# Kernel optimization log

Hardware: AMD Instinct MI355X
Metric: run time of the kernel (lower is better)

The kernel has to match this reference:

```python
import jax, jax.numpy as jnp
import numpy as np

LRELU_SLOPE = 0.2  # PyG GATConv default negative_slope
LN_EPS = 1e-5


def _layer_norm(x, g, b):
    mu = x.mean(-1, keepdims=True)
    var = x.var(-1, keepdims=True)
    return (x - mu) / jnp.sqrt(var + LN_EPS) * g + b


def _gat_conv(x, src, dst, W, a_src, a_dst, bias, heads, out_c, concat):
    # PyG GATConv (eval mode, self-loops already appended to src/dst).
    N = x.shape[0]
    h = (x @ W).reshape(N, heads, out_c)            # [N,H,C]
    e_src = (h * a_src).sum(-1)                     # [N,H]
    e_dst = (h * a_dst).sum(-1)                     # [N,H]
    e = jax.nn.leaky_relu(e_src[src] + e_dst[dst], LRELU_SLOPE)  # [E,H]
    # segment softmax over incoming edges of each dst node
    m = jax.ops.segment_max(e, dst, num_segments=N)
    m = jnp.where(jnp.isfinite(m), m, 0.0)
    w = jnp.exp(e - m[dst])
    denom = jax.ops.segment_sum(w, dst, num_segments=N)
    alpha = w / (denom[dst] + 1e-16)                # [E,H]
    out = jax.ops.segment_sum(h[src] * alpha[:, :, None], dst, num_segments=N)  # [N,H,C]
    out = out.reshape(N, heads * out_c) if concat else out.mean(1)
    return out + bias


def setup_inputs() -> dict:
    key = jax.random.key(0)
    ks = jax.random.split(key, 16)
    N, E, F0, Hd, H, G = 50000, 800000, 32, 32, 4, 512
    s = 0.1
    nrm = lambda k, shape: jax.random.normal(k, shape, jnp.float32) * s
    d = {}
    d['x'] = jax.random.normal(ks[0], (N, F0), jnp.float32)
    d['edge_index'] = jax.random.randint(ks[1], (2, E), 0, N)
    d['batch'] = jnp.sort(jax.random.randint(ks[2], (N,), 0, G))
    d['num_graphs'] = G
    # layer 1: F0 -> (Hd, H heads, concat)
    d['W1'] = nrm(ks[3], (F0, H * Hd)); d['as1'] = nrm(ks[4], (H, Hd)); d['ad1'] = nrm(ks[5], (H, Hd))
    d['b1'] = jnp.zeros((H * Hd,)); d['g1'] = jnp.ones((H * Hd,)); d['be1'] = jnp.zeros((H * Hd,))
    # layer 2: H*Hd -> (Hd, H heads, concat)
    d['W2'] = nrm(ks[6], (H * Hd, H * Hd)); d['as2'] = nrm(ks[7], (H, Hd)); d['ad2'] = nrm(ks[8], (H, Hd))
    d['b2'] = jnp.zeros((H * Hd,)); d['g2'] = jnp.ones((H * Hd,)); d['be2'] = jnp.zeros((H * Hd,))
    # layer 3: H*Hd -> (Hd, 1 head, mean)
    d['W3'] = nrm(ks[9], (H * Hd, Hd)); d['as3'] = nrm(ks[10], (1, Hd)); d['ad3'] = nrm(ks[11], (1, Hd))
    d['b3'] = jnp.zeros((Hd,)); d['g3'] = jnp.ones((Hd,)); d['be3'] = jnp.zeros((Hd,))
    # classifier MLP: 2*Hd -> Hd -> Hd//2 -> 1 (torch Linear [out,in])
    d['cW1'] = nrm(ks[12], (Hd, 2 * Hd)); d['cb1'] = jnp.zeros((Hd,))
    d['cW2'] = nrm(ks[13], (Hd // 2, Hd)); d['cb2'] = jnp.zeros((Hd // 2,))
    d['cW3'] = nrm(ks[14], (1, Hd // 2)); d['cb3'] = jnp.zeros((1,))
    return d


def reference(x, edge_index, batch, num_graphs,
              W1, as1, ad1, b1, g1, be1,
              W2, as2, ad2, b2, g2, be2,
              W3, as3, ad3, b3, g3, be3,
              cW1, cb1, cW2, cb2, cW3, cb3):
    N = x.shape[0]
    loop = jnp.arange(N)
    src = jnp.concatenate([edge_index[0], loop])
    dst = jnp.concatenate([edge_index[1], loop])
    h = jax.nn.elu(_layer_norm(_gat_conv(x, src, dst, W1, as1, ad1, b1, 4, 32, True), g1, be1))
    h = jax.nn.elu(_layer_norm(_gat_conv(h, src, dst, W2, as2, ad2, b2, 4, 32, True), g2, be2))
    h = jax.nn.elu(_layer_norm(_gat_conv(h, src, dst, W3, as3, ad3, b3, 1, 32, False), g3, be3))
    cnt = jax.ops.segment_sum(jnp.ones((N,), h.dtype), batch, num_segments=num_graphs)
    x_mean = jax.ops.segment_sum(h, batch, num_segments=num_graphs) / jnp.maximum(cnt, 1.0)[:, None]
    x_max = jax.ops.segment_max(h, batch, num_segments=num_graphs)
    f = jnp.concatenate([x_mean, x_max], axis=1)        # [G, 64]
    f = jax.nn.relu(f @ cW1.T + cb1)
    f = jax.nn.relu(f @ cW2.T + cb2)
    return (f @ cW3.T + cb3).squeeze(-1)                 # [G]
```

## Files before the change

kernel.cpp:

```cpp
#include <hip/hip_runtime.h>
#include <hip/hip_fp16.h>
#include <math.h>

#define CDIV(a, b) (((a) + (b) - 1) / (b))
#define SCAN_BS 1024
#define NBUK 512
#define ATILE 4096

typedef _Float16 f16x8 __attribute__((ext_vector_type(8)));
typedef float f32x4 __attribute__((ext_vector_type(4)));

__device__ __forceinline__ unsigned encf(float v) {
    unsigned u = __float_as_uint(v);
    return (u & 0x80000000u) ? ~u : (u | 0x80000000u);
}
__device__ __forceinline__ float decf(unsigned k) {
    unsigned u = (k & 0x80000000u) ? (k ^ 0x80000000u) : ~k;
    return __uint_as_float(u);
}

__device__ __forceinline__ float lrelu(float v) {
    return v > 0.f ? v : 0.2f * v;
}

__global__ __launch_bounds__(256) void gemm_kernel(
    const float* __restrict__ X, const float* __restrict__ W,
    float* __restrict__ Y, int M, int K, int Nout) {
    int idx = blockIdx.x * blockDim.x + threadIdx.x;
    if (idx >= M * Nout) return;
    int row = idx / Nout;
    int col = idx - row * Nout;
    const float* xr = X + (size_t)row * K;
    const float* wc = W + col;
    float acc = 0.f;
    for (int k = 0; k < K; k += 4) {
        float4 xv = *(const float4*)(xr + k);
        acc += xv.x * wc[(size_t)(k + 0) * Nout];
        acc += xv.y * wc[(size_t)(k + 1) * Nout];
        acc += xv.z * wc[(size_t)(k + 2) * Nout];
        acc += xv.w * wc[(size_t)(k + 3) * Nout];
    }
    Y[idx] = acc;
}

__device__ __forceinline__ void wprep_one(const float* __restrict__ W,
                                          __half* __restrict__ Whf, int K,
                                          int NOUT, int idx) {
    int NK = K / 32;
    int l = idx & 63, f = idx >> 6;
    int ks = f % NK, tt = f / NK;
    int quad = l >> 4, c15 = l & 15;
    _Float16 v[8];
#pragma unroll
    for (int j = 0; j < 8; ++j) {
        int k = ks * 32 + quad * 8 + j;
        int n = tt * 16 + c15;
        v[j] = (_Float16)W[(size_t)k * NOUT + n];
    }
    *(uint4*)(Whf + (size_t)idx * 8) = *(uint4*)v;
}

__device__ __forceinline__ void wprep_one_lds(const float* __restrict__ W,
                                              __half* Whf, int K, int NOUT,
                                              int idx) {
    int NK = K / 32;
    int l = idx & 63, f = idx >> 6;
    int ks = f % NK, tt = f / NK;
    int quad = l >> 4, c15 = l & 15;
    _Float16 v[8];
#pragma unroll
    for (int j = 0; j < 8; ++j) {
        int k = ks * 32 + quad * 8 + j;
        int n = tt * 16 + c15;
        v[j] = (_Float16)W[(size_t)k * NOUT + n];
    }
    *(uint4*)(Whf + (size_t)idx * 8) = *(uint4*)v;
}

__device__ __forceinline__ f16x8 loadA(const float* p) {
    float4 lo = *(const float4*)p;
    float4 hi = *(const float4*)(p + 4);
    f16x8 a;
    a[0] = (_Float16)lo.x; a[1] = (_Float16)lo.y;
    a[2] = (_Float16)lo.z; a[3] = (_Float16)lo.w;
    a[4] = (_Float16)hi.x; a[5] = (_Float16)hi.y;
    a[6] = (_Float16)hi.z; a[7] = (_Float16)hi.w;
    return a;
}
__device__ __forceinline__ f16x8 loadA(const __half* p) {
    return *(const f16x8*)p;
}

template <int K, int NOUT, int HH, typename XT, typename BP>
__device__ __forceinline__ void gemm_attn_body(
    const XT* __restrict__ X, const BP* bp, __half* __restrict__ Y,
    const float* __restrict__ a_src, const float* __restrict__ a_dst,
    float* __restrict__ es, float* __restrict__ ed, int M, int blk) {
    constexpr int NK = K / 32, NT = NOUT / 16;
    static_assert(NT == 2 * HH, "32 channels per head assumed");
    int wave = threadIdx.x >> 6, lane = threadIdx.x & 63;
    int quad = lane >> 4, c15 = lane & 15;
    int row0 = (blk * 4 + wave) * 16;
    if (row0 >= M) return;
    int arow = row0 + c15;
    if (arow >= M) arow = M - 1;
    const XT* xr = X + (size_t)arow * K + quad * 8;
    f32x4 acc[NT];
#pragma unroll
    for (int t = 0; t < NT; ++t) {
        acc[t][0] = 0.f; acc[t][1] = 0.f; acc[t][2] = 0.f; acc[t][3] = 0.f;
    }
#pragma unroll
    for (int ks = 0; ks < NK; ++ks) {
        f16x8 a = loadA(xr + ks * 32);
#pragma unroll
        for (int t = 0; t < NT; ++t) {
            f16x8 b = *(const f16x8*)&bp[((t * NK + ks) * 64 + lane) * 8];
            acc[t] = __builtin_amdgcn_mfma_f32_16x16x32_f16(a, b, acc[t],
                                                            0, 0, 0);
        }
    }
#pragma unroll
    for (int r = 0; r < 4; ++r) {
        int row = row0 + quad * 4 + r;
        if (row < M) {
#pragma unroll
            for (int t = 0; t < NT; ++t)
                Y[(size_t)row * NOUT + t * 16 + c15] = (__half)acc[t][r];
        }
    }
    float asv[NT], adv[NT];
#pragma unroll
    for (int t = 0; t < NT; ++t) {
        asv[t] = a_src[t * 16 + c15];
        adv[t] = a_dst[t * 16 + c15];
    }
#pragma unroll
    for (int h = 0; h < HH; ++h) {
#pragma unroll
        for (int r = 0; r < 4; ++r) {
            float s = acc[2 * h][r] * asv[2 * h] +
                      acc[2 * h + 1][r] * asv[2 * h + 1];
            float dd = acc[2 * h][r] * adv[2 * h] +
                       acc[2 * h + 1][r] * adv[2 * h + 1];
#pragma unroll
            for (int off = 8; off >= 1; off >>= 1) {
                s += __shfl_xor(s, off);
                dd += __shfl_xor(dd, off);
            }
            int row = row0 + quad * 4 + r;
            if (row < M) {
                if (c15 == 0) es[row * HH + h] = s;
                if (c15 == 1) ed[row * HH + h] = dd;
            }
        }
    }
}

template <int K, int NOUT, int HH, typename XT>
__global__ __launch_bounds__(256) void gemm_mfma_attn(
    const XT* __restrict__ X, const __half* __restrict__ Whf,
    __half* __restrict__ Y, const float* __restrict__ a_src,
    const float* __restrict__ a_dst, float* __restrict__ es,
    float* __restrict__ ed, int M) {
    gemm_attn_body<K, NOUT, HH>(X, Whf, Y, a_src, a_dst, es, ed, M,
                                blockIdx.x);
}

__global__ __launch_bounds__(256) void binA1_kernel(
    const int* __restrict__ ei, int E, int* __restrict__ ghist,
    int* __restrict__ pool0, int poolN, const float* __restrict__ W1,
    const float* __restrict__ W2, const float* __restrict__ W3,
    __half* __restrict__ wh2, __half* __restrict__ wh3,
    int* __restrict__ rowptr, int N, int nhist, int nwp,
    const float* __restrict__ x, __half* __restrict__ Qh,
    const float* __restrict__ as1, const float* __restrict__ ad1,
    float* __restrict__ es, float* __restrict__ ed) {
    __shared__ int lh[NBUK];
    __shared__ __half wlds[512 * 8];
    int t = threadIdx.x;
    if (blockIdx.x >= nhist + nwp) {
        for (int i = t; i < 512; i += 256)
            wprep_one_lds(W1, wlds, 32, 128, i);
        __syncthreads();
        gemm_attn_body<32, 128, 4>(x, wlds, Qh, as1, ad1, es, ed, N,
                                   blockIdx.x - nhist - nwp);
        return;
    }
    if (blockIdx.x >= nhist) {
        int idx = (blockIdx.x - nhist) * 256 + t;
        if (idx == 0) rowptr[N] = E + N;
        if (idx < 2048) {
            wprep_one(W2, wh2, 128, 128, idx);
        } else if (idx < 2560) {
            wprep_one(W3, wh3, 128, 32, idx - 2048);
        }
        return;
    }
    int gid = blockIdx.x * 256 + t;
    if (gid < poolN) pool0[gid] = 0;
    for (int i = t; i < NBUK; i += 256) lh[i] = 0;
    __syncthreads();
    int base = blockIdx.x * ATILE;
#pragma unroll 4
    for (int j = 0; j < ATILE / 256; ++j) {
        int idx = base + t + 256 * j;
        if (idx < E) atomicAdd(&lh[ei[E + idx] >> 7], 1);
    }
    __syncthreads();
    int* gh = ghist + (size_t)blockIdx.x * NBUK;
    for (int i = t; i < NBUK; i += 256) gh[i] = lh[i];
}

__global__ __launch_bounds__(64) void binA2a_kernel(
    int* __restrict__ ghist, int* __restrict__ tot, int nblk) {
    int b = blockIdx.x;
    int lane = threadIdx.x;
    int accb = 0;
    for (int chunk = 0; chunk < nblk; chunk += 64) {
        int i = chunk + lane;
        int v = (i < nblk) ? ghist[(size_t)i * NBUK + b] : 0;
        int s = v;
        for (int off = 1; off < 64; off <<= 1) {
            int tv = __shfl_up(s, off);
            if (lane >= off) s += tv;
        }
        if (i < nblk) ghist[(size_t)i * NBUK + b] = s - v + accb;
        accb += __shfl(s, 63);
    }
    if (lane == 0) tot[b] = accb;
}

__device__ __forceinline__ void bucketScan(const int* __restrict__ tot,
                                           int* __restrict__ sc, int t,
                                           int& a0, int& a1, int& excl) {
    a0 = tot[2 * t];
    a1 = tot[2 * t + 1];
    int pair = a0 + a1;
    sc[t] = pair;
    __syncthreads();
#pragma unroll
    for (int off = 1; off < 256; off <<= 1) {
        int v = (t >= off) ? sc[t - off] : 0;
        __syncthreads();
        sc[t] += v;
        __syncthreads();
    }
    excl = sc[t] - pair;
}

__global__ __launch_bounds__(256) void binA3_kernel(
    const int* __restrict__ ei, int E, const int* __restrict__ ghist,
    const int* __restrict__ tot, unsigned* __restrict__ ebuf) {
    __shared__ int lcur[NBUK];
    __shared__ int sc[256];
    int t = threadIdx.x;
    int a0, a1, excl;
    bucketScan(tot, sc, t, a0, a1, excl);
    const int* gh = ghist + (size_t)blockIdx.x * NBUK;
    lcur[2 * t] = gh[2 * t] + excl;
    lcur[2 * t + 1] = gh[2 * t + 1] + excl + a0;
    __syncthreads();
    int base = blockIdx.x * ATILE;
#pragma unroll 4
    for (int j = 0; j < ATILE / 256; ++j) {
        int idx = base + t + 256 * j;
        if (idx < E) {
            int s = ei[idx];
            int d = ei[E + idx];
            int pos = atomicAdd(&lcur[d >> 7], 1);
            ebuf[pos] = ((unsigned)d << 16) | (unsigned)s;
        }
    }
}

__global__ __launch_bounds__(256) void binB_kernel(
    const unsigned* __restrict__ ebuf, const int* __restrict__ tot,
    int* __restrict__ rowptr, int* __restrict__ csrc, int N) {
    __shared__ int cnt_[128];
    __shared__ int pre[128];
    __shared__ int lcur[128];
    __shared__ int sc[256];
    __shared__ int begS;
    int b = blockIdx.x;
    int t = threadIdx.x;
    int n0 = b << 7;
    int totb = tot[b];
    if (t < 128) cnt_[t] = 0;
    int a0, a1, excl;
    bucketScan(tot, sc, t, a0, a1, excl);
    if (t == (b >> 1)) begS = (b & 1) ? (excl + a0) : excl;
    __syncthreads();
    int beg = begS, end = begS + totb;
    for (int i = beg + t; i < end; i += 256)
        atomicAdd(&cnt_[(ebuf[i] >> 16) - n0], 1);
    __syncthreads();
    if (t < 128) pre[t] = (n0 + t < N) ? (cnt_[t] + 1) : 0;
    __syncthreads();
    for (int off = 1; off < 128; off <<= 1) {
        int v = 0;
        if (t < 128 && t >= off) v = pre[t - off];
        __syncthreads();
        if (t < 128) pre[t] += v;
        __syncthreads();
    }
    int cbase = beg + n0;
    if (t < 128 && n0 + t < N) {
        int ex = pre[t] - (cnt_[t] + 1);
        int rp = cbase + ex;
        rowptr[n0 + t] = rp;
        csrc[rp] = n0 + t;
        lcur[t] = rp + 1;
    }
    __syncthreads();
    for (int i = beg + t; i < end; i += 256) {
        unsigned e = ebuf[i];
        int d = (int)(e >> 16) - n0;
        int s = (int)(e & 0xFFFFu);
        int pos = atomicAdd(&lcur[d], 1);
        csrc[pos] = s;
    }
}

__global__ __launch_bounds__(256) void attn_kernel(
    const float* __restrict__ h, const float* __restrict__ a_src,
    const float* __restrict__ a_dst, float* __restrict__ es,
    float* __restrict__ ed, int N, int H, int C) {
    int idx = blockIdx.x * blockDim.x + threadIdx.x;
    if (idx >= N * H) return;
    int n = idx / H;
    int hh = idx - n * H;
    const float* hp = h + (size_t)n * H * C + (size_t)hh * C;
    const float* ap = a_src + hh * C;
    const float* bp = a_dst + hh * C;
    float s = 0.f, d = 0.f;
    for (int c = 0; c < C; c += 4) {
        float4 hv = *(const float4*)(hp + c);
        float4 av = *(const float4*)(ap + c);
        float4 bv = *(const float4*)(bp + c);
        s += hv.x * av.x + hv.y * av.y + hv.z * av.z + hv.w * av.w;
        d += hv.x * bv.x + hv.y * bv.y + hv.z * bv.z + hv.w * bv.w;
    }
    es[idx] = s;
    ed[idx] = d;
}

__global__ __launch_bounds__(256) void deg_kernel(const int* __restrict__ ei,
                                                  int E,
                                                  int* __restrict__ deg) {
    int e = blockIdx.x * blockDim.x + threadIdx.x;
    if (e >= E) return;
    atomicAdd(&deg[ei[E + e]], 1);
}

__global__ __launch_bounds__(SCAN_BS) void scan1_kernel(
    const int* __restrict__ deg, int* __restrict__ rowptr,
    int* __restrict__ bsum, int N) {
    __shared__ int tmp[SCAN_BS];
    int tid = threadIdx.x;
    int gid = blockIdx.x * SCAN_BS + tid;
    int v = (gid < N) ? (deg[gid] + 1) : 0;
    tmp[tid] = v;
    __syncthreads();
    for (int off = 1; off < SCAN_BS; off <<= 1) {
        int t = (tid >= off) ? tmp[tid - off] : 0;
        __syncthreads();
        tmp[tid] += t;
        __syncthreads();
    }
    if (gid < N) rowptr[gid] = tmp[tid] - v;
    if (tid == SCAN_BS - 1) bsum[blockIdx.x] = tmp[tid];
}

__global__ void scan2_kernel(int* __restrict__ bsum, int nb) {
    if (threadIdx.x == 0 && blockIdx.x == 0) {
        int acc = 0;
        for (int i = 0; i < nb; ++i) {
            int t = bsum[i];
            bsum[i] = acc;
            acc += t;
        }
    }
}

__global__ __launch_bounds__(SCAN_BS) void scan3_kernel(
    int* __restrict__ rowptr, int* __restrict__ cursor,
    int* __restrict__ csrc, const int* __restrict__ bsum, int N, int total) {
    int gid = blockIdx.x * SCAN_BS + threadIdx.x;
    if (gid < N) {
        int v = rowptr[gid] + bsum[blockIdx.x];
        rowptr[gid] = v;
        cursor[gid] = v + 1;
        csrc[v] = gid;
    }
    if (gid == 0) rowptr[N] = total;
}

__global__ __launch_bounds__(256) void scatter_kernel(
    const int* __restrict__ ei, int E, int* __restrict__ cursor,
    int* __restrict__ csrc) {
    int e = blockIdx.x * blockDim.x + threadIdx.x;
    if (e >= E) return;
    int s = ei[e];
    int d = ei[E + e];
    int pos = atomicAdd(&cursor[d], 1);
    csrc[pos] = s;
}

__global__ __launch_bounds__(256) void aggr_ln128_kernel(
    const int* __restrict__ rowptr, const int* __restrict__ csrc,
    const __half* __restrict__ h, const float* __restrict__ es,
    const float* __restrict__ ed, const float* __restrict__ bias,
    const float* __restrict__ gam, const float* __restrict__ bet,
    __half* __restrict__ outp, int N) {
    constexpr int D = 128, H = 4;
    int d = (blockIdx.x * blockDim.x + threadIdx.x) >> 4;
    int cl = threadIdx.x & 15;
    if (d >= N) return;
    int c = cl * 8;
    int hh = cl >> 2;
    float edv = ed[d * H + hh];
    float acc[8];
#pragma unroll
    for (int i = 0; i < 8; ++i) acc[i] = 0.f;
    float l = 0.f;
    int k = rowptr[d], end = rowptr[d + 1];
    for (; k + 8 <= end; k += 8) {
        int s[8];
#pragma unroll
        for (int j = 0; j < 8; ++j) s[j] = csrc[k + j];
        float e[8];
#pragma unroll
        for (int j = 0; j < 8; ++j) e[j] = es[s[j] * H + hh];
        uint4 u[8];
#pragma unroll
        for (int j = 0; j < 8; ++j)
            u[j] = *(const uint4*)(h + (size_t)s[j] * D + c);
#pragma unroll
        for (int j = 0; j < 8; ++j) {
            float w = __expf(lrelu(e[j] + edv));
            l += w;
            const __half2* hp = (const __half2*)&u[j];
#pragma unroll
            for (int i = 0; i < 4; ++i) {
                float2 f = __half22float2(hp[i]);
                acc[2 * i] += w * f.x;
                acc[2 * i + 1] += w * f.y;
            }
        }
    }
    for (; k + 4 <= end; k += 4) {
        int s[4];
#pragma unroll
        for (int j = 0; j < 4; ++j) s[j] = csrc[k + j];
        float e[4];
#pragma unroll
        for (int j = 0; j < 4; ++j) e[j] = es[s[j] * H + hh];
        uint4 u[4];
#pragma unroll
        for (int j = 0; j < 4; ++j)
            u[j] = *(const uint4*)(h + (size_t)s[j] * D + c);
#pragma unroll
        for (int j = 0; j < 4; ++j) {
            float w = __expf(lrelu(e[j] + edv));
            l += w;
            const __half2* hp = (const __half2*)&u[j];
#pragma unroll
            for (int i = 0; i < 4; ++i) {
                float2 f = __half22float2(hp[i]);
                acc[2 * i] += w * f.x;
                acc[2 * i + 1] += w * f.y;
            }
        }
    }
    for (; k < end; ++k) {
        int s = csrc[k];
        float w = __expf(lrelu(es[s * H + hh] + edv));
        uint4 u = *(const uint4*)(h + (size_t)s * D + c);
        l += w;
        const __half2* hp = (const __half2*)&u;
#pragma unroll
        for (int i = 0; i < 4; ++i) {
            float2 f = __half22float2(hp[i]);
            acc[2 * i] += w * f.x;
            acc[2 * i + 1] += w * f.y;
        }
    }
    float rl = 1.f / (l + 1e-16f);
    float4 b0 = *(const float4*)(bias + c);
    float4 b1 = *(const float4*)(bias + c + 4);
    float v[8];
    v[0] = acc[0] * rl + b0.x; v[1] = acc[1] * rl + b0.y;
    v[2] = acc[2] * rl + b0.z; v[3] = acc[3] * rl + b0.w;
    v[4] = acc[4] * rl + b1.x; v[5] = acc[5] * rl + b1.y;
    v[6] = acc[6] * rl + b1.z; v[7] = acc[7] * rl + b1.w;
    float sm = 0.f, ssum = 0.f;
#pragma unroll
    for (int i = 0; i < 8; ++i) { sm += v[i]; ssum += v[i] * v[i]; }
#pragma unroll
    for (int off = 1; off <= 8; off <<= 1) {
        sm += __shfl_xor(sm, off);
        ssum += __shfl_xor(ssum, off);
    }
    float mean = sm / D;
    float var = ssum / D - mean * mean;
    float rstd = rsqrtf(var + 1e-5f);
    float4 g0 = *(const float4*)(gam + c);
    float4 g1 = *(const float4*)(gam + c + 4);
    float4 t0 = *(const float4*)(bet + c);
    float4 t1 = *(const float4*)(bet + c + 4);
    float gv[8] = {g0.x, g0.y, g0.z, g0.w, g1.x, g1.y, g1.z, g1.w};
    float tv[8] = {t0.x, t0.y, t0.z, t0.w, t1.x, t1.y, t1.z, t1.w};
    __half2 p[4];
#pragma unroll
    for (int i = 0; i < 4; ++i) {
        float o0 = (v[2 * i] - mean) * rstd * gv[2 * i] + tv[2 * i];
        float o1 = (v[2 * i + 1] - mean) * rstd * gv[2 * i + 1] + tv[2 * i + 1];
        o0 = o0 > 0.f ? o0 : expm1f(o0);
        o1 = o1 > 0.f ? o1 : expm1f(o1);
        p[i] = __floats2half2_rn(o0, o1);
    }
    uint4 uo;
    uo.x = *(unsigned*)&p[0];
    uo.y = *(unsigned*)&p[1];
    uo.z = *(unsigned*)&p[2];
    uo.w = *(unsigned*)&p[3];
    *(uint4*)(outp + (size_t)d * D + c) = uo;
}

__global__ __launch_bounds__(256) void aggr_ln32_pool_kernel(
    const int* __restrict__ rowptr, const int* __restrict__ csrc,
    const __half* __restrict__ h, const float* __restrict__ es,
    const float* __restrict__ ed, const float* __restrict__ bias,
    const float* __restrict__ gam, const float* __restrict__ bet,
    const int* __restrict__ batch, float* __restrict__ psum,
    unsigned* __restrict__ pmax, float* __restrict__ cnt, int N) {
    constexpr int D = 32;
    __shared__ float lsum[2][32];
    __shared__ unsigned lmax[2][32];
    __shared__ float lcnt[2];
    __shared__ int g0s;
    int tid = threadIdx.x;
    int d = (blockIdx.x * 256 + tid) >> 3;
    int cl = tid & 7;
    int c = cl * 4;
    int dbase = blockIdx.x * 32;
    if (tid < 64) {
        lsum[tid >> 5][tid & 31] = 0.f;
        lmax[tid >> 5][tid & 31] = 0u;
    }
    if (tid < 2) lcnt[tid] = 0.f;
    if (tid == 0) g0s = batch[dbase < N ? dbase : (N - 1)];
    __syncthreads();
    int g0 = g0s;
    if (d < N) {
        float edv = ed[d];
        float acc[4] = {0.f, 0.f, 0.f, 0.f};
        float l = 0.f;
        int k = rowptr[d], end = rowptr[d + 1];
        for (; k + 8 <= end; k += 8) {
            int s[8];
#pragma unroll
            for (int j = 0; j < 8; ++j) s[j] = csrc[k + j];
            float e[8];
#pragma unroll
            for (int j = 0; j < 8; ++j) e[j] = es[s[j]];
            uint2 u[8];
#pragma unroll
            for (int j = 0; j < 8; ++j)
                u[j] = *(const uint2*)(h + (size_t)s[j] * D + c);
#pragma unroll
            for (int j = 0; j < 8; ++j) {
                float w = __expf(lrelu(e[j] + edv));
                l += w;
                float2 f0 = __half22float2(*(__half2*)&u[j].x);
                float2 f1 = __half22float2(*(__half2*)&u[j].y);
                acc[0] += w * f0.x; acc[1] += w * f0.y;
                acc[2] += w * f1.x; acc[3] += w * f1.y;
            }
        }
        for (; k + 4 <= end; k += 4) {
            int s[4];
#pragma unroll
            for (int j = 0; j < 4; ++j) s[j] = csrc[k + j];
            float e[4];
#pragma unroll
            for (int j = 0; j < 4; ++j) e[j] = es[s[j]];
            uint2 u[4];
#pragma unroll
            for (int j = 0; j < 4; ++j)
                u[j] = *(const uint2*)(h + (size_t)s[j] * D + c);
#pragma unroll
            for (int j = 0; j < 4; ++j) {
                float w = __expf(lrelu(e[j] + edv));
                l += w;
                float2 f0 = __half22float2(*(__half2*)&u[j].x);
                float2 f1 = __half22float2(*(__half2*)&u[j].y);
                acc[0] += w * f0.x; acc[1] += w * f0.y;
                acc[2] += w * f1.x; acc[3] += w * f1.y;
            }
        }
        for (; k < end; ++k) {
            int s = csrc[k];
            float w = __expf(lrelu(es[s] + edv));
            uint2 u = *(const uint2*)(h + (size_t)s * D + c);
            l += w;
            float2 f0 = __half22float2(*(__half2*)&u.x);
            float2 f1 = __half22float2(*(__half2*)&u.y);
            acc[0] += w * f0.x; acc[1] += w * f0.y;
            acc[2] += w * f1.x; acc[3] += w * f1.y;
        }
        float rl = 1.f / (l + 1e-16f);
        float4 b4 = *(const float4*)(bias + c);
        float v0 = acc[0] * rl + b4.x;
        float v1 = acc[1] * rl + b4.y;
        float v2 = acc[2] * rl + b4.z;
        float v3 = acc[3] * rl + b4.w;
        float sm = v0 + v1 + v2 + v3;
        float ssum = v0 * v0 + v1 * v1 + v2 * v2 + v3 * v3;
#pragma unroll
        for (int off = 1; off <= 4; off <<= 1) {
            sm += __shfl_xor(sm, off);
            ssum += __shfl_xor(ssum, off);
        }
        float mean = sm / D;
        float var = ssum / D - mean * mean;
        float rstd = rsqrtf(var + 1e-5f);
        float4 g4 = *(const float4*)(gam + c);
        float4 t4 = *(const float4*)(bet + c);
        float o0 = (v0 - mean) * rstd * g4.x + t4.x;
        float o1 = (v1 - mean) * rstd * g4.y + t4.y;
        float o2 = (v2 - mean) * rstd * g4.z + t4.z;
        float o3 = (v3 - mean) * rstd * g4.w + t4.w;
        o0 = o0 > 0.f ? o0 : expm1f(o0);
        o1 = o1 > 0.f ? o1 : expm1f(o1);
        o2 = o2 > 0.f ? o2 : expm1f(o2);
        o3 = o3 > 0.f ? o3 : expm1f(o3);
        int g = batch[d];
        int goff = g - g0;
        if (goff >= 0 && goff < 2) {
            atomicAdd(&lsum[goff][c + 0], o0);
            atomicAdd(&lsum[goff][c + 1], o1);
            atomicAdd(&lsum[goff][c + 2], o2);
            atomicAdd(&lsum[goff][c + 3], o3);
            atomicMax(&lmax[goff][c + 0], encf(o0));
            atomicMax(&lmax[goff][c + 1], encf(o1));
            atomicMax(&lmax[goff][c + 2], encf(o2));
            atomicMax(&lmax[goff][c + 3], encf(o3));
            if (cl == 0) atomicAdd(&lcnt[goff], 1.0f);
        } else {
            atomicAdd(&psum[g * D + c + 0], o0);
            atomicAdd(&psum[g * D + c + 1], o1);
            atomicAdd(&psum[g * D + c + 2], o2);
            atomicAdd(&psum[g * D + c + 3], o3);
            atomicMax(&pmax[g * D + c + 0], encf(o0));
            atomicMax(&pmax[g * D + c + 1], encf(o1));
            atomicMax(&pmax[g * D + c + 2], encf(o2));
            atomicMax(&pmax[g * D + c + 3], encf(o3));
            if (cl == 0) atomicAdd(&cnt[g], 1.0f);
        }
    }
    __syncthreads();
    if (tid < 64) {
        int go = tid >> 5, cc = tid & 31;
        unsigned m = lmax[go][cc];
        if (m != 0u) {
            int gg = g0 + go;
            atomicAdd(&psum[gg * D + cc], lsum[go][cc]);
            atomicMax(&pmax[gg * D + cc], m);
            if (cc == 0) atomicAdd(&cnt[gg], lcnt[go]);
        }
    }
}

__global__ __launch_bounds__(256) void aggr_csr_kernel(
    const int* __restrict__ rowptr, const int* __restrict__ csrc,
    const float* __restrict__ h, const float* __restrict__ es,
    const float* __restrict__ ed, float* __restrict__ outp, int N, int H,
    int C) {
    int D = H * C;
    int wave = (blockIdx.x * blockDim.x + threadIdx.x) >> 6;
    int lane = threadIdx.x & 63;
    if (wave >= N) return;
    int d = wave;
    int c0 = lane, c1 = lane + 64;
    bool a0 = c0 < D, a1 = c1 < D;
    int h0 = a0 ? c0 / C : 0;
    int h1 = a1 ? c1 / C : 0;
    float edv0 = a0 ? ed[d * H + h0] : 0.f;
    float edv1 = a1 ? ed[d * H + h1] : 0.f;
    float m0 = -INFINITY, m1 = -INFINITY;
    float l0 = 0.f, l1 = 0.f, acc0 = 0.f, acc1 = 0.f;
    int beg = rowptr[d], end = rowptr[d + 1];
    for (int k = beg; k < end; ++k) {
        int s = csrc[k];
        const float* hp = h + (size_t)s * D;
        if (a0) {
            float v = lrelu(es[s * H + h0] + edv0);
            float nm = fmaxf(m0, v);
            float sc = __expf(m0 - nm);
            float w = __expf(v - nm);
            l0 = l0 * sc + w;
            acc0 = acc0 * sc + w * hp[c0];
            m0 = nm;
        }
        if (a1) {
            float v = lrelu(es[s * H + h1] + edv1);
            float nm = fmaxf(m1, v);
            float sc = __expf(m1 - nm);
            float w = __expf(v - nm);
            l1 = l1 * sc + w;
            acc1 = acc1 * sc + w * hp[c1];
            m1 = nm;
        }
    }
    if (a0) outp[(size_t)d * D + c0] = acc0 / (l0 + 1e-16f);
    if (a1) outp[(size_t)d * D + c1] = acc1 / (l1 + 1e-16f);
}

__global__ __launch_bounds__(64) void ln_elu_kernel(
    const float* __restrict__ in, const float* __restrict__ bias,
    const float* __restrict__ gam, const float* __restrict__ bet,
    float* __restrict__ outp, int D) {
    int n = blockIdx.x;
    int lane = threadIdx.x;
    int c0 = lane, c1 = lane + 64;
    bool a0 = c0 < D, a1 = c1 < D;
    float v0 = 0.f, v1 = 0.f;
    if (a0) v0 = in[(size_t)n * D + c0] + bias[c0];
    if (a1) v1 = in[(size_t)n * D + c1] + bias[c1];
    float s = v0 + v1;
    float ss = v0 * v0 + v1 * v1;
    for (int off = 32; off; off >>= 1) {
        s += __shfl_xor(s, off);
        ss += __shfl_xor(ss, off);
    }
    float mean = s / D;
    float var = ss / D - mean * mean;
    float rstd = rsqrtf(var + 1e-5f);
    if (a0) {
        float o = (v0 - mean) * rstd * gam[c0] + bet[c0];
        outp[(size_t)n * D + c0] = o > 0.f ? o : expm1f(o);
    }
    if (a1) {
        float o = (v1 - mean) * rstd * gam[c1] + bet[c1];
        outp[(size_t)n * D + c1] = o > 0.f ? o : expm1f(o);
    }
}

__global__ __launch_bounds__(256) void pool_kernel(
    const float* __restrict__ h, const int* __restrict__ batch, int N, int C,
    float* __restrict__ psum, unsigned* __restrict__ pmax,
    float* __restrict__ cnt) {
    int idx = blockIdx.x * blockDim.x + threadIdx.x;
    if (idx >= N * C) return;
    int n = idx / C;
    int c = idx - n * C;
    int g = batch[n];
    float v = h[(size_t)n * C + c];
    atomicAdd(&psum[g * C + c], v);
    atomicMax(&pmax[g * C + c], encf(v));
    if (c == 0) atomicAdd(&cnt[g], 1.0f);
}

__global__ __launch_bounds__(64) void mlp_kernel(
    const float* __restrict__ psum, const unsigned* __restrict__ pmax,
    const float* __restrict__ cnt, const float* __restrict__ cW1,
    const float* __restrict__ cb1, const float* __restrict__ cW2,
    const float* __restrict__ cb2, const float* __restrict__ cW3,
    const float* __restrict__ cb3, float* __restrict__ outp, int C) {
    __shared__ float f[64];
    __shared__ float t1[32];
    __shared__ float t2[16];
    int g = blockIdx.x;
    int t = threadIdx.x;
    float c = fmaxf(cnt[g], 1.0f);
    if (t < C) {
        f[t] = psum[g * C + t] / c;
    } else if (t < 2 * C) {
        unsigned k = pmax[g * C + (t - C)];
        f[t] = (k == 0u) ? -INFINITY : decf(k);
    }
    __syncthreads();
    if (t < 32) {
        float a = cb1[t];
        for (int i = 0; i < 64; ++i) a += f[i] * cW1[t * 64 + i];
        t1[t] = fmaxf(a, 0.f);
    }
    __syncthreads();
    if (t < 16) {
        float a = cb2[t];
        for (int i = 0; i < 32; ++i) a += t1[i] * cW2[t * 32 + i];
        t2[t] = fmaxf(a, 0.f);
    }
    __syncthreads();
    if (t == 0) {
        float a = cb3[0];
        for (int i = 0; i < 16; ++i) a += t2[i] * cW3[i];
        outp[g] = a;
    }
}

extern "C" void kernel_launch(void* const* d_in, const int* in_sizes, int n_in,
                              void* d_out, int out_size, void* d_ws,
                              size_t ws_size, hipStream_t stream) {
    const float* x = (const float*)d_in[0];
    const int* ei = (const int*)d_in[1];
    const int* batch = (const int*)d_in[2];
    const float* W1 = (const float*)d_in[4];
    const float* as1 = (const float*)d_in[5];
    const float* ad1 = (const float*)d_in[6];
    const float* b1 = (const float*)d_in[7];
    const float* g1 = (const float*)d_in[8];
    const float* be1 = (const float*)d_in[9];
    const float* W2 = (const float*)d_in[10];
    const float* as2 = (const float*)d_in[11];
    const float* ad2 = (const float*)d_in[12];
    const float* b2 = (const float*)d_in[13];
    const float* g2 = (const float*)d_in[14];
    const float* be2 = (const float*)d_in[15];
    const float* W3 = (const float*)d_in[16];
    const float* as3 = (const float*)d_in[17];
    const float* ad3 = (const float*)d_in[18];
    const float* b3 = (const float*)d_in[19];
    const float* g3 = (const float*)d_in[20];
    const float* be3 = (const float*)d_in[21];
    const float* cW1 = (const float*)d_in[22];
    const float* cb1 = (const float*)d_in[23];
    const float* cW2 = (const float*)d_in[24];
    const float* cb2 = (const float*)d_in[25];
    const float* cW3 = (const float*)d_in[26];
    const float* cb3 = (const float*)d_in[27];

    const int N = in_sizes[2];
    const int E = in_sizes[1] / 2;
    const int F0 = in_sizes[0] / N;
    const int Hd = in_sizes[19];
    const int H = in_sizes[5] / Hd;
    const int D = H * Hd;
    const int H3 = in_sizes[17] / Hd;
    const int G = out_size;
    const int EN = E + N;
    const bool shapes_ok = (F0 == 32 && Hd == 32 && H == 4 && D == 128 &&
                            H3 == 1 && N <= 65536);

    char* w = (char*)d_ws;
    size_t off = 0;
    auto carve = [&](size_t bytes) -> void* {
        void* p = w + off;
        off = (off + bytes + 255) & ~(size_t)255;
        return p;
    };
    float* Q = (float*)carve((size_t)N * D * 4);
    __half* Qh = (__half*)Q;
    float* R = (float*)carve((size_t)N * D * 4);
    float* P = (float*)carve((size_t)N * D * 4);
    __half* Ph = (__half*)P;
    float* es = (float*)carve((size_t)N * H * 4);
    float* ed = (float*)carve((size_t)N * H * 4);
    int* rowptr = (int*)carve((size_t)(N + 1) * 4);
    int* cursor = (int*)carve((size_t)N * 4);
    int* csrc = (int*)carve((size_t)EN * 4);
    int* bsum = (int*)carve((size_t)CDIV(N, SCAN_BS) * 4);
    const int nblkA = CDIV(E, ATILE);
    int* ghist = (int*)carve((size_t)nblkA * NBUK * 4);
    int* tot = (int*)carve((size_t)NBUK * 4);
    unsigned* ebuf = (unsigned*)carve((size_t)E * 4);
    __half* wh2 = (__half*)carve((size_t)8 * 4 * 64 * 8 * 2);
    __half* wh3 = (__half*)carve((size_t)2 * 4 * 64 * 8 * 2);
    float* psum = (float*)carve((size_t)G * Hd * 4);
    unsigned* pmax = (unsigned*)carve((size_t)G * Hd * 4);
    float* cnt = (float*)carve((size_t)G * 4);
    (void)ws_size;
    (void)n_in;

    const int BLK = 256;
    const int nb = CDIV(N, SCAN_BS);
    const int poolInts = G * Hd * 2 + G;

    if (shapes_ok) {
        const int nwp = 10;
        const int ngemm1 = CDIV(N, 64);
        binA1_kernel<<<nblkA + nwp + ngemm1, 256, 0, stream>>>(
            ei, E, ghist, (int*)psum, poolInts, W1, W2, W3, wh2, wh3,
            rowptr, N, nblkA, nwp, x, Qh, as1, ad1, es, ed);
        binA2a_kernel<<<NBUK, 64, 0, stream>>>(ghist, tot, nblkA);
        binA3_kernel<<<nblkA, 256, 0, stream>>>(ei, E, ghist, tot, ebuf);
        binB_kernel<<<CDIV(N, 128), 256, 0, stream>>>(ebuf, tot, rowptr,
                                                      csrc, N);
        aggr_ln128_kernel<<<CDIV(N, 16), 256, 0, stream>>>(
            rowptr, csrc, Qh, es, ed, b1, g1, be1, Ph, N);
        gemm_mfma_attn<128, 128, 4, __half><<<CDIV(N, 64), 256, 0, stream>>>(
            Ph, wh2, Qh, as2, ad2, es, ed, N);
        aggr_ln128_kernel<<<CDIV(N, 16), 256, 0, stream>>>(
            rowptr, csrc, Qh, es, ed, b2, g2, be2, Ph, N);
        gemm_mfma_attn<128, 32, 1, __half><<<CDIV(N, 64), 256, 0, stream>>>(
            Ph, wh3, Qh, as3, ad3, es, ed, N);
        aggr_ln32_pool_kernel<<<CDIV(N, 32), 256, 0, stream>>>(
            rowptr, csrc, Qh, es, ed, b3, g3, be3, batch, psum, pmax, cnt, N);
    } else {
        hipMemsetAsync(psum, 0, (size_t)G * Hd * 4, stream);
        hipMemsetAsync(pmax, 0, (size_t)G * Hd * 4, stream);
        hipMemsetAsync(cnt, 0, (size_t)G * 4, stream);
        hipMemsetAsync(cursor, 0, (size_t)N * 4, stream);
        deg_kernel<<<CDIV(E, BLK), BLK, 0, stream>>>(ei, E, cursor);
        scan1_kernel<<<nb, SCAN_BS, 0, stream>>>(cursor, rowptr, bsum, N);
        scan2_kernel<<<1, 64, 0, stream>>>(bsum, nb);
        scan3_kernel<<<nb, SCAN_BS, 0, stream>>>(rowptr, cursor, csrc, bsum, N, EN);
        scatter_kernel<<<CDIV(E, BLK), BLK, 0, stream>>>(ei, E, cursor, csrc);
        gemm_kernel<<<CDIV(N * D, BLK), BLK, 0, stream>>>(x, W1, Q, N, F0, D);
        attn_kernel<<<CDIV(N * H, BLK), BLK, 0, stream>>>(Q, as1, ad1, es, ed, N, H, Hd);
        aggr_csr_kernel<<<CDIV(N, 4), BLK, 0, stream>>>(rowptr, csrc, Q, es, ed, R, N, H, Hd);
        ln_elu_kernel<<<N, 64, 0, stream>>>(R, b1, g1, be1, P, D);
        gemm_kernel<<<CDIV(N * D, BLK), BLK, 0, stream>>>(P, W2, Q, N, D, D);
        attn_kernel<<<CDIV(N * H, BLK), BLK, 0, stream>>>(Q, as2, ad2, es, ed, N, H, Hd);
        aggr_csr_kernel<<<CDIV(N, 4), BLK, 0, stream>>>(rowptr, csrc, Q, es, ed, R, N, H, Hd);
        ln_elu_kernel<<<N, 64, 0, stream>>>(R, b2, g2, be2, P, D);
        gemm_kernel<<<CDIV(N * Hd, BLK), BLK, 0, stream>>>(P, W3, Q, N, D, Hd);
        attn_kernel<<<CDIV(N * H3, BLK), BLK, 0, stream>>>(Q, as3, ad3, es, ed, N, H3, Hd);
        aggr_csr_kernel<<<CDIV(N, 4), BLK, 0, stream>>>(rowptr, csrc, Q, es, ed, R, N, H3, Hd);
        ln_elu_kernel<<<N, 64, 0, stream>>>(R, b3, g3, be3, P, Hd);
        pool_kernel<<<CDIV(N * Hd, BLK), BLK, 0, stream>>>(P, batch, N, Hd, psum, pmax, cnt);
    }

    mlp_kernel<<<G, 64, 0, stream>>>(psum, pmax, cnt, cW1, cb1, cW2, cb2, cW3,
                                     cb3, (float*)d_out, Hd);
}
```

Baseline: 273.1 us.

## Fuse GAT aggregation+LayerNorm+ELU with following MFMA GEMM and attention-logit kernel

Merges each layer's aggregation, LayerNorm and ELU kernel with the next layer's MFMA projection and attention-logit computation. A 16-row tile of normalized activations is staged in LDS and multiplied straight away, so the intermediate fp16 activation no longer goes through global memory and two launches are removed. Separate es/ed buffers are double-buffered because the fused kernel reads one layer's logits while writing the next. The cost is an extra LDS barrier, smaller GEMM tiles (16 rows instead of 64) with repeated weight reads per block, and idle waves in the 32-output case.

```diff
diff --git a/kernel.cpp b/kernel.cpp
--- a/kernel.cpp
+++ b/kernel.cpp
@@ -155,16 +155,6 @@
             }
         }
     }
-}
-
-template <int K, int NOUT, int HH, typename XT>
-__global__ __launch_bounds__(256) void gemm_mfma_attn(
-    const XT* __restrict__ X, const __half* __restrict__ Whf,
-    __half* __restrict__ Y, const float* __restrict__ a_src,
-    const float* __restrict__ a_dst, float* __restrict__ es,
-    float* __restrict__ ed, int M) {
-    gemm_attn_body<K, NOUT, HH>(X, Whf, Y, a_src, a_dst, es, ed, M,
-                                blockIdx.x);
 }
 
 __global__ __launch_bounds__(256) void binA1_kernel(
@@ -407,40 +397,86 @@
     csrc[pos] = s;
 }
 
-__global__ __launch_bounds__(256) void aggr_ln128_kernel(
+template <int NOUT, int HH>
+__global__ __launch_bounds__(256) void aggr_gemm_kernel(
     const int* __restrict__ rowptr, const int* __restrict__ csrc,
     const __half* __restrict__ h, const float* __restrict__ es,
     const float* __restrict__ ed, const float* __restrict__ bias,
     const float* __restrict__ gam, const float* __restrict__ bet,
-    __half* __restrict__ outp, int N) {
+    const __half* __restrict__ Whf, __half* __restrict__ Y,
+    const float* __restrict__ a_src, const float* __restrict__ a_dst,
+    float* __restrict__ es_o, float* __restrict__ ed_o, int N) {
     constexpr int D = 128, H = 4;
-    int d = (blockIdx.x * blockDim.x + threadIdx.x) >> 4;
-    int cl = threadIdx.x & 15;
-    if (d >= N) return;
+    constexpr int NK = 4, NT = NOUT / 16;
+    static_assert(NT == 2 * HH, "32 channels per head assumed");
+    __shared__ __half lds[16][136];
+    int tid = threadIdx.x;
+    int r = tid >> 4;
+    int cl = tid & 15;
+    int d = blockIdx.x * 16 + r;
     int c = cl * 8;
-    int hh = cl >> 2;
-    float edv = ed[d * H + hh];
-    float acc[8];
-#pragma unroll
-    for (int i = 0; i < 8; ++i) acc[i] = 0.f;
-    float l = 0.f;
-    int k = rowptr[d], end = rowptr[d + 1];
-    for (; k + 8 <= end; k += 8) {
-        int s[8];
-#pragma unroll
-        for (int j = 0; j < 8; ++j) s[j] = csrc[k + j];
-        float e[8];
-#pragma unroll
-        for (int j = 0; j < 8; ++j) e[j] = es[s[j] * H + hh];
-        uint4 u[8];
-#pragma unroll
-        for (int j = 0; j < 8; ++j)
-            u[j] = *(const uint4*)(h + (size_t)s[j] * D + c);
-#pragma unroll
-        for (int j = 0; j < 8; ++j) {
-            float w = __expf(lrelu(e[j] + edv));
+    if (d < N) {
+        int hh = cl >> 2;
+        float edv = ed[d * H + hh];
+        float acc[8];
+#pragma unroll
+        for (int i = 0; i < 8; ++i) acc[i] = 0.f;
+        float l = 0.f;
+        int k = rowptr[d], end = rowptr[d + 1];
+        for (; k + 8 <= end; k += 8) {
+            int s[8];
+#pragma unroll
+            for (int j = 0; j < 8; ++j) s[j] = csrc[k + j];
+            float e[8];
+#pragma unroll
+            for (int j = 0; j < 8; ++j) e[j] = es[s[j] * H + hh];
+            uint4 u[8];
+#pragma unroll
+            for (int j = 0; j < 8; ++j)
+                u[j] = *(const uint4*)(h + (size_t)s[j] * D + c);
+#pragma unroll
+            for (int j = 0; j < 8; ++j) {
+                float w = __expf(lrelu(e[j] + edv));
+                l += w;
+                const __half2* hp = (const __half2*)&u[j];
+#pragma unroll
+                for (int i = 0; i < 4; ++i) {
+                    float2 f = __half22float2(hp[i]);
+                    acc[2 * i] += w * f.x;
+                    acc[2 * i + 1] += w * f.y;
+                }
+            }
+        }
+        for (; k + 4 <= end; k += 4) {
+            int s[4];
+#pragma unroll
+            for (int j = 0; j < 4; ++j) s[j] = csrc[k + j];
+            float e[4];
+#pragma unroll
+            for (int j = 0; j < 4; ++j) e[j] = es[s[j] * H + hh];
+            uint4 u[4];
+#pragma unroll
+            for (int j = 0; j < 4; ++j)
+                u[j] = *(const uint4*)(h + (size_t)s[j] * D + c);
+#pragma unroll
+            for (int j = 0; j < 4; ++j) {
+                float w = __expf(lrelu(e[j] + edv));
+                l += w;
+                const __half2* hp = (const __half2*)&u[j];
+#pragma unroll
+                for (int i = 0; i < 4; ++i) {
+                    float2 f = __half22float2(hp[i]);
+                    acc[2 * i] += w * f.x;
+                    acc[2 * i + 1] += w * f.y;
+                }
+            }
+        }
+        for (; k < end; ++k) {
+            int s = csrc[k];
+            float w = __expf(lrelu(es[s * H + hh] + edv));
+            uint4 u = *(const uint4*)(h + (size_t)s * D + c);
             l += w;
-            const __half2* hp = (const __half2*)&u[j];
+            const __half2* hp = (const __half2*)&u;
 #pragma unroll
             for (int i = 0; i < 4; ++i) {
                 float2 f = __half22float2(hp[i]);
@@ -448,84 +484,98 @@
                 acc[2 * i + 1] += w * f.y;
             }
         }
-    }
-    for (; k + 4 <= end; k += 4) {
-        int s[4];
-#pragma unroll
-        for (int j = 0; j < 4; ++j) s[j] = csrc[k + j];
-        float e[4];
-#pragma unroll
-        for (int j = 0; j < 4; ++j) e[j] = es[s[j] * H + hh];
-        uint4 u[4];
-#pragma unroll
-        for (int j = 0; j < 4; ++j)
-            u[j] = *(const uint4*)(h + (size_t)s[j] * D + c);
-#pragma unroll
-        for (int j = 0; j < 4; ++j) {
-            float w = __expf(lrelu(e[j] + edv));
-            l += w;
-            const __half2* hp = (const __half2*)&u[j];
-#pragma unroll
-            for (int i = 0; i < 4; ++i) {
-                float2 f = __half22float2(hp[i]);
-                acc[2 * i] += w * f.x;
-                acc[2 * i + 1] += w * f.y;
+        float rl = 1.f / (l + 1e-16f);
+        float4 b0 = *(const float4*)(bias + c);
+        float4 b1 = *(const float4*)(bias + c + 4);
+        float v[8];
+        v[0] = acc[0] * rl + b0.x; v[1] = acc[1] * rl + b0.y;
+        v[2] = acc[2] * rl + b0.z; v[3] = acc[3] * rl + b0.w;
+        v[4] = acc[4] * rl + b1.x; v[5] = acc[5] * rl + b1.y;
+        v[6] = acc[6] * rl + b1.z; v[7] = acc[7] * rl + b1.w;
+        float sm = 0.f, ssum = 0.f;
+#pragma unroll
+        for (int i = 0; i < 8; ++i) { sm += v[i]; ssum += v[i] * v[i]; }
+#pragma unroll
+        for (int off = 1; off <= 8; off <<= 1) {
+            sm += __shfl_xor(sm, off);
+            ssum += __shfl_xor(ssum, off);
+        }
+        float mean = sm / D;
+        float var = ssum / D - mean * mean;
+        float rstd = rsqrtf(var + 1e-5f);
+        float4 g0 = *(const float4*)(gam + c);
+        float4 g1 = *(const float4*)(gam + c + 4);
+        float4 t0 = *(const float4*)(bet + c);
+        float4 t1 = *(const float4*)(bet + c + 4);
+        float gv[8] = {g0.x, g0.y, g0.z, g0.w, g1.x, g1.y, g1.z, g1.w};
+        float tv[8] = {t0.x, t0.y, t0.z, t0.w, t1.x, t1.y, t1.z, t1.w};
+        __half2 p[4];
+#pragma unroll
+        for (int i = 0; i < 4; ++i) {
+            float o0 = (v[2 * i] - mean) * rstd * gv[2 * i] + tv[2 * i];
+            float o1 = (v[2 * i + 1] - mean) * rstd * gv[2 * i + 1] +
+                       tv[2 * i + 1];
+            o0 = o0 > 0.f ? o0 : expm1f(o0);
+            o1 = o1 > 0.f ? o1 : expm1f(o1);
+            p[i] = __floats2half2_rn(o0, o1);
+        }
+        uint4 uo;
+        uo.x = *(unsigned*)&p[0];
+        uo.y = *(unsigned*)&p[1];
+        uo.z = *(unsigned*)&p[2];
+        uo.w = *(unsigned*)&p[3];
+        *(uint4*)&lds[r][c] = uo;
+    } else {
+        uint4 z = {0u, 0u, 0u, 0u};
+        *(uint4*)&lds[r][c] = z;
+    }
+    __syncthreads();
+    int wave = tid >> 6, lane = tid & 63;
+    int quad = lane >> 4, c15 = lane & 15;
+    int row0 = blockIdx.x * 16;
+    int t0 = (NT == 8) ? 2 * wave : 0;
+    bool act = (NT == 8) || (wave == 0);
+    if (act) {
+        f32x4 a0c, a1c;
+        a0c[0] = 0.f; a0c[1] = 0.f; a0c[2] = 0.f; a0c[3] = 0.f;
+        a1c = a0c;
+#pragma unroll
+        for (int ks = 0; ks < NK; ++ks) {
+            f16x8 a = *(f16x8*)&lds[c15][quad * 8 + ks * 32];
+            f16x8 b0 = *(const f16x8*)(Whf +
+                        (size_t)((t0 * NK + ks) * 64 + lane) * 8);
+            f16x8 b1 = *(const f16x8*)(Whf +
+                        (size_t)(((t0 + 1) * NK + ks) * 64 + lane) * 8);
+            a0c = __builtin_amdgcn_mfma_f32_16x16x32_f16(a, b0, a0c, 0, 0, 0);
+            a1c = __builtin_amdgcn_mfma_f32_16x16x32_f16(a, b1, a1c, 0, 0, 0);
+        }
+#pragma unroll
+        for (int rr = 0; rr < 4; ++rr) {
+            int row = row0 + quad * 4 + rr;
+            if (row < N) {
+                Y[(size_t)row * NOUT + t0 * 16 + c15] = (__half)a0c[rr];
+                Y[(size_t)row * NOUT + (t0 + 1) * 16 + c15] = (__half)a1c[rr];
             }
         }
-    }
-    for (; k < end; ++k) {
-        int s = csrc[k];
-        float w = __expf(lrelu(es[s * H + hh] + edv));
-        uint4 u = *(const uint4*)(h + (size_t)s * D + c);
-        l += w;
-        const __half2* hp = (const __half2*)&u;
-#pragma unroll
-        for (int i = 0; i < 4; ++i) {
-            float2 f = __half22float2(hp[i]);
-            acc[2 * i] += w * f.x;
-            acc[2 * i + 1] += w * f.y;
-        }
-    }
-    float rl = 1.f / (l + 1e-16f);
-    float4 b0 = *(const float4*)(bias + c);
-    float4 b1 = *(const float4*)(bias + c + 4);
-    float v[8];
-    v[0] = acc[0] * rl + b0.x; v[1] = acc[1] * rl + b0.y;
-    v[2] = acc[2] * rl + b0.z; v[3] = acc[3] * rl + b0.w;
-    v[4] = acc[4] * rl + b1.x; v[5] = acc[5] * rl + b1.y;
-    v[6] = acc[6] * rl + b1.z; v[7] = acc[7] * rl + b1.w;
-    float sm = 0.f, ssum = 0.f;
-#pragma unroll
-    for (int i = 0; i < 8; ++i) { sm += v[i]; ssum += v[i] * v[i]; }
-#pragma unroll
-    for (int off = 1; off <= 8; off <<= 1) {
-        sm += __shfl_xor(sm, off);
-        ssum += __shfl_xor(ssum, off);
-    }
-    float mean = sm / D;
-    float var = ssum / D - mean * mean;
-    float rstd = rsqrtf(var + 1e-5f);
-    float4 g0 = *(const float4*)(gam + c);
-    float4 g1 = *(const float4*)(gam + c + 4);
-    float4 t0 = *(const float4*)(bet + c);
-    float4 t1 = *(const float4*)(bet + c + 4);
-    float gv[8] = {g0.x, g0.y, g0.z, g0.w, g1.x, g1.y, g1.z, g1.w};
-    float tv[8] = {t0.x, t0.y, t0.z, t0.w, t1.x, t1.y, t1.z, t1.w};
-    __half2 p[4];
-#pragma unroll
-    for (int i = 0; i < 4; ++i) {
-        float o0 = (v[2 * i] - mean) * rstd * gv[2 * i] + tv[2 * i];
-        float o1 = (v[2 * i + 1] - mean) * rstd * gv[2 * i + 1] + tv[2 * i + 1];
-        o0 = o0 > 0.f ? o0 : expm1f(o0);
-        o1 = o1 > 0.f ? o1 : expm1f(o1);
-        p[i] = __floats2half2_rn(o0, o1);
-    }
-    uint4 uo;
-    uo.x = *(unsigned*)&p[0];
-    uo.y = *(unsigned*)&p[1];
-    uo.z = *(unsigned*)&p[2];
-    uo.w = *(unsigned*)&p[3];
-    *(uint4*)(outp + (size_t)d * D + c) = uo;
+        int hd = t0 >> 1;
+        float as0 = a_src[t0 * 16 + c15], as1 = a_src[(t0 + 1) * 16 + c15];
+        float ad0 = a_dst[t0 * 16 + c15], ad1 = a_dst[(t0 + 1) * 16 + c15];
+#pragma unroll
+        for (int rr = 0; rr < 4; ++rr) {
+            float s = a0c[rr] * as0 + a1c[rr] * as1;
+            float dd = a0c[rr] * ad0 + a1c[rr] * ad1;
+#pragma unroll
+            for (int off = 8; off >= 1; off >>= 1) {
+                s += __shfl_xor(s, off);
+                dd += __shfl_xor(dd, off);
+            }
+            int row = row0 + quad * 4 + rr;
+            if (row < N) {
+                if (c15 == 0) es_o[row * HH + hd] = s;
+                if (c15 == 1) ed_o[row * HH + hd] = dd;
+            }
+        }
+    }
 }
 
 __global__ __launch_bounds__(256) void aggr_ln32_pool_kernel(
@@ -856,8 +906,10 @@
     float* R = (float*)carve((size_t)N * D * 4);
     float* P = (float*)carve((size_t)N * D * 4);
     __half* Ph = (__half*)P;
-    float* es = (float*)carve((size_t)N * H * 4);
-    float* ed = (float*)carve((size_t)N * H * 4);
+    float* es1 = (float*)carve((size_t)N * H * 4);
+    float* ed1 = (float*)carve((size_t)N * H * 4);
+    float* es2 = (float*)carve((size_t)N * H * 4);
+    float* ed2 = (float*)carve((size_t)N * H * 4);
     int* rowptr = (int*)carve((size_t)(N + 1) * 4);
     int* cursor = (int*)carve((size_t)N * 4);
     int* csrc = (int*)carve((size_t)EN * 4);
@@ -883,22 +935,23 @@
         const int ngemm1 = CDIV(N, 64);
         binA1_kernel<<<nblkA + nwp + ngemm1, 256, 0, stream>>>(
             ei, E, ghist, (int*)psum, poolInts, W1, W2, W3, wh2, wh3,
-            rowptr, N, nblkA, nwp, x, Qh, as1, ad1, es, ed);
+            rowptr, N, nblkA, nwp, x, Qh, as1, ad1, es1, ed1);
         binA2a_kernel<<<NBUK, 64, 0, stream>>>(ghist, tot, nblkA);
         binA3_kernel<<<nblkA, 256, 0, stream>>>(ei, E, ghist, tot, ebuf);
         binB_kernel<<<CDIV(N, 128), 256, 0, stream>>>(ebuf, tot, rowptr,
                                                       csrc, N);
-        aggr_ln128_kernel<<<CDIV(N, 16), 256, 0, stream>>>(
-            rowptr, csrc, Qh, es, ed, b1, g1, be1, Ph, N);
-        gemm_mfma_attn<128, 128, 4, __half><<<CDIV(N, 64), 256, 0, stream>>>(
-            Ph, wh2, Qh, as2, ad2, es, ed, N);
-        aggr_ln128_kernel<<<CDIV(N, 16), 256, 0, stream>>>(
-            rowptr, csrc, Qh, es, ed, b2, g2, be2, Ph, N);
-        gemm_mfma_attn<128, 32, 1, __half><<<CDIV(N, 64), 256, 0, stream>>>(
-            Ph, wh3, Qh, as3, ad3, es, ed, N);
+        aggr_gemm_kernel<128, 4><<<CDIV(N, 16), 256, 0, stream>>>(
+            rowptr, csrc, Qh, es1, ed1, b1, g1, be1, wh2, Ph, as2, ad2,
+            es2, ed2, N);
+        aggr_gemm_kernel<32, 1><<<CDIV(N, 16), 256, 0, stream>>>(
+            rowptr, csrc, Ph, es2, ed2, b2, g2, be2, wh3, Qh, as3, ad3,
+            es1, ed1, N);
         aggr_ln32_pool_kernel<<<CDIV(N, 32), 256, 0, stream>>>(
-            rowptr, csrc, Qh, es, ed, b3, g3, be3, batch, psum, pmax, cnt, N);
+            rowptr, csrc, Qh, es1, ed1, b3, g3, be3, batch, psum, pmax,
+            cnt, N);
     } else {
+        float* es = es1;
+        float* ed = ed1;
         hipMemsetAsync(psum, 0, (size_t)G * Hd * 4, stream);
         hipMemsetAsync(pmax, 0, (size_t)G * Hd * 4, stream);
         hipMemsetAsync(cnt, 0, (size_t)G * 4, stream);
```

Result: faster. 264.0 us, median of 2 (-3.3%).
